# Optimization experiments

Hardware: AMD Instinct MI355X
Metric: run time of the kernel (lower is better)

The kernel has to match this reference:

```python
import jax, jax.numpy as jnp
import numpy as np
from jax import lax

B = 8192
HS = 64        # hidden_size (output channels)
HS4 = HS + 4   # internal channel count (68)
K = 3          # conv kernel size


def setup_inputs() -> dict:
    key = jax.random.key(0)
    ks = jax.random.split(key, 16)
    def n(k, shape, s=1.0):
        return jax.random.normal(k, shape, dtype=jnp.float32) * s
    return {
        "x": n(ks[0], (B, HS, 6, 6)),
        "cell": n(ks[1], (B, 2)),
        "interspace_coord": n(ks[2], (B, 2, 6, 6)),
        "conv1_w": n(ks[3], (HS4, HS4, K, K), 0.05),
        "conv1_b": n(ks[4], (HS4,), 0.05),
        "conv3_w": n(ks[5], (HS4, HS4, K, K), 0.05),
        "conv3_b": n(ks[6], (HS4,), 0.05),
        "lin5_w": n(ks[7], (9 * HS, HS4 * 25), 0.02),
        "lin5_b": n(ks[8], (9 * HS,), 0.02),
        "lin4_w": n(ks[9], (9 * HS, HS4 * 16), 0.02),
        "lin4_b": n(ks[10], (9 * HS,), 0.02),
        "lin3_w": n(ks[11], (9 * HS, HS4 * 9), 0.02),
        "lin3_b": n(ks[12], (9 * HS,), 0.02),
        "final_w": n(ks[13], (HS, 9 * HS), 0.02),
        "final_b": n(ks[14], (HS,), 0.02),
    }


def _conv(z, w, b):
    # torch Conv2d with padding=k//2, stride 1 == SAME conv, NCHW/OIHW
    y = lax.conv_general_dilated(z, w, (1, 1), 'SAME',
                                 dimension_numbers=('NCHW', 'OIHW', 'NCHW'))
    return y + b[None, :, None, None]


def _corners(z, ws):
    # four corner windows, stacked on a new leading axis (corner-major)
    H, W = z.shape[-2:]
    return jnp.stack([z[..., :ws, :ws],
                      z[..., :ws, W - ws:],
                      z[..., H - ws:, :ws],
                      z[..., H - ws:, W - ws:]], axis=0)


def reference(x, cell, interspace_coord,
              conv1_w, conv1_b, conv3_w, conv3_b,
              lin5_w, lin5_b, lin4_w, lin4_b, lin3_w, lin3_b,
              final_w, final_b):
    Bn = x.shape[0]
    new_cell = jnp.broadcast_to(cell.reshape(Bn, -1)[:, :, None, None],
                                (Bn, 2, 6, 6))
    lins = {5: (lin5_w, lin5_b), 4: (lin4_w, lin4_b), 3: (lin3_w, lin3_b)}
    for ws in (5, 4, 3):
        z = jnp.concatenate([x, new_cell, interspace_coord], axis=1)  # [B,68,6,6]
        z = _corners(z, ws).reshape(-1, HS4, ws, ws)                  # [4B,68,ws,ws]
        z = jnp.sin(z) + jnp.cos(z)
        z = jax.nn.relu(_conv(z, conv1_w, conv1_b))
        z = jnp.sin(z) + jnp.cos(z)
        z = jax.nn.relu(_conv(z, conv3_w, conv3_b)).reshape(4, Bn, -1)
        Wl, bl = lins[ws]
        z = jax.nn.relu(z @ Wl.T + bl).reshape(4, Bn, HS, 3, 3)
        m = jnp.concatenate([z[0], z[1]], axis=-1)   # [B,64,3,6]
        n = jnp.concatenate([z[2], z[3]], axis=-1)
        x = jnp.concatenate([m, n], axis=-2)          # [B,64,6,6]
    ew = 3
    c = _corners(x, ew)                               # [4,B,64,3,3]
    c = c.reshape(4 * Bn, -1) @ final_w.T + final_b   # [4B,64]
    c = c.reshape(Bn, HS, 2, 2)                       # same flat-order reshape as torch
    xc = x[:, :, ew - 1:ew + 1, ew - 1:ew + 1]        # center 2x2
    return (xc * c).reshape(Bn, HS, -1)
```

## Files before the change

kernel.cpp:

```cpp
#include <hip/hip_runtime.h>
#include <hip/hip_bf16.h>
#include <cstdint>
#include <cstddef>

#define BN 8192
#define MTOT 32768

using bf16 = __hip_bfloat16;
typedef float f32x4 __attribute__((ext_vector_type(4)));
typedef short short8 __attribute__((ext_vector_type(8)));

__device__ __forceinline__ bf16 f2b(float v) { return __float2bfloat16(v); }
__device__ __forceinline__ float b2f(bf16 v) { return __bfloat162float(v); }
__device__ __forceinline__ float sincos_sum(float x) {
    return 1.41421356237f * __sinf(x + 0.78539816340f);
}


__global__ __launch_bounds__(256)
void zprep_block(const float* __restrict__ xF, const float* __restrict__ cell,
                 const float* __restrict__ isc, bf16* __restrict__ Z,
                 int m0g, int CM)
{
    constexpr int KD = 1728, KTRUE = 1700;
    const int b = blockIdx.x, tid = threadIdx.x;
    __shared__ float s[68][37];

    for (int i = tid; i < 64 * 36; i += 256) {
        int ic = i / 36, off = i % 36;
        s[ic][off] = sincos_sum(xF[((size_t)b * 64 + ic) * 36 + off]);
    }
    if (tid < 2) {
        float t = sincos_sum(cell[b * 2 + tid]);
        #pragma unroll
        for (int off = 0; off < 36; off++) s[64 + tid][off] = t;
    }
    if (tid >= 64 && tid < 136) {
        int j = tid - 64;
        int ic = j / 36, off = j % 36;
        s[66 + ic][off] = sincos_sum(isc[((size_t)b * 2 + ic) * 36 + off]);
    }
    __syncthreads();

    for (int i = tid; i < 4 * KD; i += 256) {
        int q = i / KD, k = i % KD;
        int gm = q * BN + b;
        if (gm < m0g || gm >= m0g + CM) continue;
        float v = 0.f;
        if (k < KTRUE) {
            int pi = k / 68, ic = k % 68;
            int r = (q >> 1) + pi / 5;
            int c = (q & 1) + pi % 5;
            v = s[ic][r * 6 + c];
        }
        Z[(size_t)(gm - m0g) * KD + k] = f2b(v);
    }
}

template<int WSv>
__device__ __forceinline__ bf16 conv_elem(const float* __restrict__ src, int n, int k)
{
    constexpr int KTRUE = 68 * WSv * WSv;
    float v = 0.f;
    if (n < KTRUE && k < KTRUE) {
        int po = n / 68, oc = n % 68, ro = po / WSv, co = po % WSv;
        int pi = k / 68, ic = k % 68, ri = pi / WSv, ci = pi % WSv;
        int kr = ri - ro + 1, kc = ci - co + 1;
        if (kr >= 0 && kr < 3 && kc >= 0 && kc < 3)
            v = src[((oc * 68 + ic) * 3 + kr) * 3 + kc];
    }
    return f2b(v);
}
template<int WSv>
__device__ __forceinline__ bf16 lin_elem(const float* __restrict__ wl, int n, int k)
{
    constexpr int KTRUE = 68 * WSv * WSv;
    float v = 0.f;
    if (n < 576 && k < KTRUE) {
        int pi = k / 68, ic = k % 68;
        v = wl[(size_t)n * KTRUE + ic * (WSv * WSv) + pi];
    }
    return f2b(v);
}

__global__ void megabuild(const float* __restrict__ c1w, const float* __restrict__ c3w,
                          const float* __restrict__ l5w, const float* __restrict__ l4w,
                          const float* __restrict__ l3w, const float* __restrict__ fw,
                          const float* __restrict__ c1b, const float* __restrict__ c3b,
                          const float* __restrict__ bl5, const float* __restrict__ bl4,
                          const float* __restrict__ bl3, const float* __restrict__ bfin,
                          const float* __restrict__ cell, const float* __restrict__ isc,
                          bf16* __restrict__ w1d5, bf16* __restrict__ w3d5,
                          bf16* __restrict__ w1d4, bf16* __restrict__ w3d4,
                          bf16* __restrict__ w1d3, bf16* __restrict__ w3d3,
                          bf16* __restrict__ wl5p, bf16* __restrict__ wl4p,
                          bf16* __restrict__ wl3p, bf16* __restrict__ wfp,
                          float* __restrict__ bias,
                          bf16* __restrict__ Z4, bf16* __restrict__ Z3)
{
    constexpr unsigned S0 = 2u*1792*1728, S1 = 2u*1152*1088, S2 = 2u*640*640;
    constexpr unsigned S3 = 640u*1728, S4 = 640u*1088, S5 = 640u*640;
    constexpr unsigned S6 = 128u*576, S7 = 9216;
    constexpr unsigned S8 = 4u*8192*16*4, S9 = 4u*8192*9*4, S10 = 32768u*28;
    constexpr unsigned O1=S0, O2=O1+S1, O3=O2+S2, O4=O3+S3, O5=O4+S4, O6=O5+S5,
                       O7=O6+S6, O8=O7+S7, O9=O8+S8, O10=O9+S9, OT=O10+S10;
    unsigned e = blockIdx.x * 256u + threadIdx.x;
    if (e >= OT) return;
    if (e < O1) {
        constexpr unsigned per = 1792u*1728;
        unsigned i = (e < per) ? e : e - per;
        bf16* dst = (e < per) ? w1d5 : w3d5;
        const float* src = (e < per) ? c1w : c3w;
        dst[i] = conv_elem<5>(src, (int)(i / 1728u), (int)(i % 1728u));
    } else if (e < O2) {
        unsigned i0 = e - O1; constexpr unsigned per = 1152u*1088;
        unsigned i = (i0 < per) ? i0 : i0 - per;
        bf16* dst = (i0 < per) ? w1d4 : w3d4;
        const float* src = (i0 < per) ? c1w : c3w;
        dst[i] = conv_elem<4>(src, (int)(i / 1088u), (int)(i % 1088u));
    } else if (e < O3) {
        unsigned i0 = e - O2; constexpr unsigned per = 640u*640;
        unsigned i = (i0 < per) ? i0 : i0 - per;
        bf16* dst = (i0 < per) ? w1d3 : w3d3;
        const float* src = (i0 < per) ? c1w : c3w;
        dst[i] = conv_elem<3>(src, (int)(i / 640u), (int)(i % 640u));
    } else if (e < O4) {
        unsigned i = e - O3;
        wl5p[i] = lin_elem<5>(l5w, (int)(i / 1728u), (int)(i % 1728u));
    } else if (e < O5) {
        unsigned i = e - O4;
        wl4p[i] = lin_elem<4>(l4w, (int)(i / 1088u), (int)(i % 1088u));
    } else if (e < O6) {
        unsigned i = e - O5;
        wl3p[i] = lin_elem<3>(l3w, (int)(i / 640u), (int)(i % 640u));
    } else if (e < O7) {
        unsigned i = e - O6, n = i / 576u, k = i % 576u;
        wfp[i] = (n < 64u) ? f2b(fw[n * 576u + k]) : f2b(0.f);
    } else if (e < O8) {
        int i = (int)(e - O7);
        float v = 0.f;
        if (i < 1792)      { int n = i;        if (n < 1700) v = c1b[n % 68]; }
        else if (i < 3584) { int n = i - 1792; if (n < 1700) v = c3b[n % 68]; }
        else if (i < 4736) { int n = i - 3584; if (n < 1088) v = c1b[n % 68]; }
        else if (i < 5888) { int n = i - 4736; if (n < 1088) v = c3b[n % 68]; }
        else if (i < 6528) { int n = i - 5888; if (n < 612)  v = c1b[n % 68]; }
        else if (i < 7168) { int n = i - 6528; if (n < 612)  v = c3b[n % 68]; }
        else if (i < 7808) { int n = i - 7168; if (n < 576)  v = bl5[n]; }
        else if (i < 8448) { int n = i - 7808; if (n < 576)  v = bl4[n]; }
        else if (i < 9088) { int n = i - 8448; if (n < 576)  v = bl3[n]; }
        else               { int n = i - 9088; if (n < 64)   v = bfin[n]; }
        bias[i] = v;
    } else if (e < O9) {
        unsigned i = e - O8;
        int j = (int)(i & 3u); i >>= 2;
        int pi = (int)(i & 15u); i >>= 4;
        int b = (int)(i & 8191u); int q = (int)(i >> 13);
        float t;
        if (j < 2) t = cell[b * 2 + j];
        else {
            int r = (q >> 1) * 2 + pi / 4, c = (q & 1) * 2 + pi % 4;
            t = isc[((size_t)b * 2 + (j - 2)) * 36 + r * 6 + c];
        }
        Z4[((size_t)q * BN + b) * 1088 + pi * 68 + 64 + j] = f2b(sincos_sum(t));
    } else if (e < O10) {
        unsigned i = e - O9;
        int j = (int)(i & 3u); i >>= 2;
        int pi = (int)(i % 9u); i /= 9u;
        int b = (int)(i & 8191u); int q = (int)(i >> 13);
        float t;
        if (j < 2) t = cell[b * 2 + j];
        else {
            int r = (q >> 1) * 3 + pi / 3, c = (q & 1) * 3 + pi % 3;
            t = isc[((size_t)b * 2 + (j - 2)) * 36 + r * 6 + c];
        }
        Z3[((size_t)q * BN + b) * 640 + pi * 68 + 64 + j] = f2b(sincos_sum(t));
    } else {
        unsigned i = e - O10;
        int m = (int)(i / 28u), t = (int)(i % 28u);
        Z3[(size_t)m * 640 + 612 + t] = f2b(0.f);
    }
}

__device__ __forceinline__ void gload_lds16(const bf16* g, const bf16* lds_wave_base)
{
    unsigned off = (unsigned)(uintptr_t)lds_wave_base;
    off = __builtin_amdgcn_readfirstlane(off);
    __builtin_amdgcn_global_load_lds((const __attribute__((address_space(1))) unsigned int*)g,
                                     (__attribute__((address_space(3))) unsigned int*)off,
                                     16, 0, 0);
}

__device__ __forceinline__ int imin(int a, int b) { return a < b ? a : b; }
__device__ __forceinline__ int imax(int a, int b) { return a > b ? a : b; }

template<int EPI, int WS, int WN>
__global__ __launch_bounds__(512, 2)
void gemm8(const bf16* __restrict__ A, const bf16* __restrict__ Bm, int KD,
           const float* __restrict__ bias, int ntiles,
           bf16* __restrict__ C, int ldc, int nlimit,
           int m0g, bf16* __restrict__ znext)
{
    __shared__ bf16 As[3][16384];
    __shared__ bf16 Bs[3][4096];
    const int tid = threadIdx.x;
    const int wave = tid >> 6, lane = tid & 63;
    const int l15 = lane & 15, lq = lane >> 4;
    const int wr = wave * 64;

    const int id = blockIdx.x;
    const int mt8 = (int)gridDim.x / (ntiles * 8);
    const int xcd = id & 7, local = id >> 3;
    const int m_idx = xcd * mt8 + local / ntiles;
    const int n_idx = local % ntiles;
    const int n0 = n_idx * 128, m0 = m_idx * 512;

    int s0b = 0, s0e = KD, s1b = 0, s1e = 0, s2b = 0, s2e = 0;
    if (WS > 0) {
        int po_lo = imin(n0 / 68, WS * WS - 1);
        int po_hi = imin((n0 + 127) / 68, WS * WS - 1);
        int ro_lo = po_lo / WS, ro_hi = po_hi / WS;
        int r_lo = imax(ro_lo - 1, 0), r_hi = imin(ro_hi + 1, WS - 1);
        int ci_lo = 0, ci_hi = WS - 1;
        if (ro_lo == ro_hi) {
            ci_lo = imax(po_lo % WS - 1, 0);
            ci_hi = imin(po_hi % WS + 1, WS - 1);
        }
        if (ci_lo == 0 && ci_hi == WS - 1) {
            s0b = (r_lo * WS * 68) & ~31;
            s0e = imin(KD, ((r_hi + 1) * WS * 68 + 31) & ~31);
        } else {
            s0b = ((r_lo * WS + ci_lo) * 68) & ~31;
            s0e = imin(KD, (((r_lo * WS + ci_hi + 1) * 68) + 31) & ~31);
            if (r_hi > r_lo) {
                s1b = (((r_lo + 1) * WS + ci_lo) * 68) & ~31;
                s1e = imin(KD, ((((r_lo + 1) * WS + ci_hi + 1) * 68) + 31) & ~31);
            }
            if (r_hi > r_lo + 1) {
                s2b = (((r_lo + 2) * WS + ci_lo) * 68) & ~31;
                s2e = imin(KD, ((((r_lo + 2) * WS + ci_hi + 1) * 68) + 31) & ~31);
            }
        }
    }
    const int c0 = (s0e - s0b) >> 5;
    const int c1 = c0 + ((s1e - s1b) >> 5);
    const int nt = c1 + ((s2e - s2b) >> 5);
    auto k0_of = [&](int t2) -> int {
        int k = s0b + (t2 << 5);
        if (t2 >= c0) k = s1b + ((t2 - c0) << 5);
        if (t2 >= c1) k = s2b + ((t2 - c1) << 5);
        return k;
    };

    const int srow = tid >> 2;
    const int sc8 = (tid & 3) ^ ((srow >> 1) & 3);
    const bf16* aSrc = A + (size_t)(m0 + srow) * KD + sc8 * 8;
    const bf16* bSrc = Bm + (size_t)(n0 + srow) * KD + sc8 * 8;
    const int sOff = srow * 32 + (tid & 3) * 8;

    auto stageA01 = [&](int k0, int buf) {
        gload_lds16(aSrc + k0, &As[buf][sOff]);
        gload_lds16(aSrc + k0 + (size_t)128 * KD, &As[buf][sOff + 4096]);
    };
    auto stageA23 = [&](int k0, int buf) {
        gload_lds16(aSrc + k0 + (size_t)256 * KD, &As[buf][sOff + 8192]);
        gload_lds16(aSrc + k0 + (size_t)384 * KD, &As[buf][sOff + 12288]);
    };
    auto stageB = [&](int k0, int buf) {
        gload_lds16(bSrc + k0, &Bs[buf][sOff]);
    };

    const int lrA = wr + l15;
    const int offA0 = lrA * 32 + ((lq ^ ((l15 >> 1) & 3)) * 8);
    const int offB0 = l15 * 32 + ((lq ^ ((l15 >> 1) & 3)) * 8);

    f32x4 acc[4][8];
    #pragma unroll
    for (int i = 0; i < 4; i++)
        #pragma unroll
        for (int j = 0; j < 8; j++) { f32x4 z = {0.f, 0.f, 0.f, 0.f}; acc[i][j] = z; }

    {
        const int k0a = k0_of(0);
        stageA01(k0a, 0); stageA23(k0a, 0); stageB(k0a, 0);
        if (nt > 1) {
            const int k0b = k0_of(1);
            stageA01(k0b, 1); stageA23(k0b, 1); stageB(k0b, 1);
        }
        __syncthreads();
    }

    for (int t = 0; t < nt; ++t) {
        const int cur = t % 3;
        const int nx = (t + 2) % 3;
        const bool pf = (t + 2) < nt;

        const bf16* Ac = &As[cur][0];
        const bf16* Bc = &Bs[cur][0];

        short8 af[4], bg[8];
        #pragma unroll
        for (int i = 0; i < 4; i++) af[i] = *(const short8*)&Ac[offA0 + i * 512];
        #pragma unroll
        for (int j = 0; j < 8; j++) bg[j] = *(const short8*)&Bc[offB0 + j * 512];

        if (pf) {
            const int k2 = k0_of(t + 2);
            stageA01(k2, nx); stageA23(k2, nx); stageB(k2, nx);
        }

        __builtin_amdgcn_s_setprio(1);
        #pragma unroll
        for (int i = 0; i < 4; i++)
            #pragma unroll
            for (int j = 0; j < 8; j++)
                acc[i][j] = __builtin_amdgcn_mfma_f32_16x16x32_bf16(af[i], bg[j], acc[i][j], 0, 0, 0);
        __builtin_amdgcn_s_setprio(0);

        if (pf) asm volatile("s_waitcnt vmcnt(5)" ::: "memory");
        else    asm volatile("s_waitcnt vmcnt(0)" ::: "memory");
        __builtin_amdgcn_s_barrier();
    }

    float bj[8];
    #pragma unroll
    for (int j = 0; j < 8; j++) bj[j] = bias[n0 + j * 16 + l15];

    #pragma unroll
    for (int i = 0; i < 4; i++) {
        #pragma unroll
        for (int j = 0; j < 8; j++) {
            int n = n0 + j * 16 + l15;
            #pragma unroll
            for (int r = 0; r < 4; r++) {
                int m = m0 + wr + i * 16 + lq * 4 + r;
                float v = acc[i][j][r];
                if (EPI == 0) {
                    if (n < nlimit) {
                        v += bj[j]; v = fmaxf(v, 0.f); v = sincos_sum(v);
                        C[(size_t)m * ldc + n] = f2b(v);
                    }
                } else if (EPI == 1) {
                    if (n < nlimit) {
                        v += bj[j]; v = fmaxf(v, 0.f);
                        C[(size_t)m * ldc + n] = f2b(v);
                    }
                } else {
                    if (n < 576) {
                        v += bj[j]; v = fmaxf(v, 0.f);
                        bf16 tv = f2b(sincos_sum(v));
                        int gm = m0g + m;
                        int q = gm >> 13, b = gm & (BN - 1);
                        int ch = n / 9, p = n % 9;
                        int R = p / 3 + (q >> 1) * 3, Cc = p % 3 + (q & 1) * 3;
                        constexpr int OFF = 6 - WN;
                        constexpr int KDN = (WN == 4) ? 1088 : 640;
                        #pragma unroll
                        for (int qr = 0; qr < 2; qr++) {
                            int rr = R - OFF * qr;
                            if (rr < 0 || rr >= WN) continue;
                            #pragma unroll
                            for (int qc = 0; qc < 2; qc++) {
                                int cc = Cc - OFF * qc;
                                if (cc < 0 || cc >= WN) continue;
                                int pi = rr * WN + cc;
                                znext[((size_t)((qr * 2 + qc) * BN + b)) * KDN + pi * 68 + ch] = tv;
                            }
                        }
                    }
                }
            }
        }
    }
}

template<int EPI, int WS, int WN>
__global__ __launch_bounds__(256)
void gemm_bt(const bf16* __restrict__ A, const bf16* __restrict__ Bm, int KD,
             const float* __restrict__ bias, int ntiles,
             bf16* __restrict__ C, int ldc, int nlimit,
             int m0g, bf16* __restrict__ znext,
             const bf16* __restrict__ afin_xc, float* __restrict__ outp)
{
    __shared__ bf16 As[128 * 32];
    __shared__ bf16 Bs[128 * 32];
    const int tid = threadIdx.x;
    const int wave = tid >> 6, lane = tid & 63;
    const int l15 = lane & 15, lq = lane >> 4;
    const int wr = (wave >> 1) * 64, wc = (wave & 1) * 64;

    const int id = blockIdx.x;
    const int mt8 = (int)gridDim.x / (ntiles * 8);
    const int xcd = id & 7, local = id >> 3;
    const int m_idx = xcd * mt8 + local / ntiles;
    const int n_idx = local % ntiles;
    const int n0 = n_idx * 128, m0 = m_idx * 128;

    int nspans = 1, sbeg[4], send[4];
    sbeg[0] = 0; send[0] = KD;
    if (WS > 0) {
        int po_lo = imin(n0 / 68, WS * WS - 1);
        int po_hi = imin((n0 + 127) / 68, WS * WS - 1);
        int ro_lo = po_lo / WS, ro_hi = po_hi / WS;
        int r_lo = imax(ro_lo - 1, 0), r_hi = imin(ro_hi + 1, WS - 1);
        int ci_lo = 0, ci_hi = WS - 1;
        if (ro_lo == ro_hi) {
            ci_lo = imax(po_lo % WS - 1, 0);
            ci_hi = imin(po_hi % WS + 1, WS - 1);
        }
        if (ci_lo == 0 && ci_hi == WS - 1) {
            sbeg[0] = (r_lo * WS * 68) & ~31;
            send[0] = imin(KD, ((r_hi + 1) * WS * 68 + 31) & ~31);
        } else {
            nspans = 0;
            for (int ri = r_lo; ri <= r_hi; ri++) {
                sbeg[nspans] = ((ri * WS + ci_lo) * 68) & ~31;
                send[nspans] = imin(KD, (((ri * WS + ci_hi + 1) * 68) + 31) & ~31);
                nspans++;
            }
        }
    }

    float bj[4];
    #pragma unroll
    for (int j = 0; j < 4; j++) bj[j] = bias[n0 + wc + j * 16 + l15];

    const bf16* Ab = A + (size_t)m0 * KD;
    const bf16* Bb = Bm + (size_t)n0 * KD;
    const int srow = tid >> 2, scol = (tid & 3) * 8;
    const bf16* aG0 = Ab + (size_t)srow * KD + scol;
    const bf16* aG1 = Ab + (size_t)(srow + 64) * KD + scol;
    const bf16* bG0 = Bb + (size_t)srow * KD + scol;
    const bf16* bG1 = Bb + (size_t)(srow + 64) * KD + scol;
    const bf16* lA0 = &As[wave * 512];
    const bf16* lA1 = &As[2048 + wave * 512];
    const bf16* lB0 = &Bs[wave * 512];
    const bf16* lB1 = &Bs[2048 + wave * 512];

    f32x4 acc[4][4];
    #pragma unroll
    for (int i = 0; i < 4; i++)
        #pragma unroll
        for (int j = 0; j < 4; j++) { f32x4 z = {0.f, 0.f, 0.f, 0.f}; acc[i][j] = z; }

    for (int s = 0; s < nspans; s++) {
        for (int k0 = sbeg[s]; k0 < send[s]; k0 += 32) {
            gload_lds16(aG0 + k0, lA0);
            gload_lds16(aG1 + k0, lA1);
            gload_lds16(bG0 + k0, lB0);
            gload_lds16(bG1 + k0, lB1);
            __syncthreads();
            short8 af[4], bg[4];
            #pragma unroll
            for (int i = 0; i < 4; i++) af[i] = *(const short8*)&As[(wr + i * 16 + l15) * 32 + lq * 8];
            #pragma unroll
            for (int j = 0; j < 4; j++) bg[j] = *(const short8*)&Bs[(wc + j * 16 + l15) * 32 + lq * 8];
            #pragma unroll
            for (int i = 0; i < 4; i++)
                #pragma unroll
                for (int j = 0; j < 4; j++)
                    acc[i][j] = __builtin_amdgcn_mfma_f32_16x16x32_bf16(af[i], bg[j], acc[i][j], 0, 0, 0);
            __syncthreads();
        }
    }

    #pragma unroll
    for (int i = 0; i < 4; i++) {
        #pragma unroll
        for (int j = 0; j < 4; j++) {
            int n = n0 + wc + j * 16 + l15;
            #pragma unroll
            for (int r = 0; r < 4; r++) {
                int m = m0 + wr + i * 16 + lq * 4 + r;
                float v = acc[i][j][r];
                if (EPI == 0) {
                    if (n < nlimit) {
                        v += bj[j]; v = fmaxf(v, 0.f); v = sincos_sum(v);
                        C[(size_t)m * ldc + n] = f2b(v);
                    }
                } else if (EPI == 1) {
                    if (n < nlimit) {
                        v += bj[j]; v = fmaxf(v, 0.f);
                        C[(size_t)m * ldc + n] = f2b(v);
                    }
                } else if (EPI == 2) {
                    if (n < 576) {
                        v += bj[j]; v = fmaxf(v, 0.f);
                        bf16 t = f2b(sincos_sum(v));
                        int gm = m0g + m;
                        int q = gm >> 13, b = gm & (BN - 1);
                        int ch = n / 9, p = n % 9;
                        int R = p / 3 + (q >> 1) * 3, Cc = p % 3 + (q & 1) * 3;
                        constexpr int OFF = 6 - WN;
                        constexpr int KDN = (WN == 4) ? 1088 : 640;
                        #pragma unroll
                        for (int qr = 0; qr < 2; qr++) {
                            int rr = R - OFF * qr;
                            if (rr < 0 || rr >= WN) continue;
                            #pragma unroll
                            for (int qc = 0; qc < 2; qc++) {
                                int cc = Cc - OFF * qc;
                                if (cc < 0 || cc >= WN) continue;
                                int pi = rr * WN + cc;
                                znext[((size_t)((qr * 2 + qc) * BN + b)) * KDN + pi * 68 + ch] = t;
                            }
                        }
                    }
                } else {
                    if (n < 64) {
                        v += bj[j];
                        int gm = m0g + m;
                        int f = gm * 64 + n;
                        int b2 = f >> 8, rem = f & 255;
                        int ch2 = rem >> 2, ii = (rem >> 1) & 1, jj = rem & 1;
                        int qq = ii * 2 + jj;
                        const int offt[4] = {8, 6, 2, 0};
                        float xc = b2f(afin_xc[((size_t)qq * BN + b2) * 576 + ch2 * 9 + offt[qq]]);
                        outp[f] = v * xc;
                    }
                }
            }
        }
    }
}

extern "C" void kernel_launch(void* const* d_in, const int* in_sizes, int n_in,
                              void* d_out, int out_size, void* d_ws, size_t ws_size,
                              hipStream_t stream)
{
    const float* x    = (const float*)d_in[0];
    const float* cell = (const float*)d_in[1];
    const float* isc  = (const float*)d_in[2];
    const float* c1w  = (const float*)d_in[3];
    const float* c1b  = (const float*)d_in[4];
    const float* c3w  = (const float*)d_in[5];
    const float* c3b  = (const float*)d_in[6];
    const float* l5w  = (const float*)d_in[7];
    const float* l5b  = (const float*)d_in[8];
    const float* l4w  = (const float*)d_in[9];
    const float* l4b  = (const float*)d_in[10];
    const float* l3w  = (const float*)d_in[11];
    const float* l3b  = (const float*)d_in[12];
    const float* fw   = (const float*)d_in[13];
    const float* fb   = (const float*)d_in[14];

    char* base = (char*)d_ws;
    size_t cur = 0;
    auto take = [&](size_t bytes) -> char* {
        char* r = base + cur; cur += (bytes + 255) & ~(size_t)255; return r;
    };

    const size_t Z4B = (size_t)MTOT * 1088 * 2;
    const size_t Z3B = (size_t)MTOT * 640 * 2;
    const size_t AFB = (size_t)MTOT * 576 * 2;
    size_t wbytes = 2 * (1792ull * 1728 + 1152ull * 1088 + 640ull * 640) * 2
                  + (640ull * 1728 + 640ull * 1088 + 640ull * 640) * 2
                  + 128ull * 576 * 2 + 9216ull * 4 + 64 * 256;
    auto need = [&](int nc) -> size_t {
        return Z4B + Z3B + AFB + wbytes + 2 * ((size_t)(MTOT / nc) * 1728 * 2);
    };
    const bool use8 = (ws_size >= need(8));
    int nchunk = use8 ? ((ws_size >= need(1)) ? 1 : (ws_size >= need(2)) ? 2
                       : (ws_size >= need(4)) ? 4 : 8)
                      : 16;

    bf16* Z4   = (bf16*)take(Z4B);
    bf16* Z3   = (bf16*)take(Z3B);
    bf16* afinb = (bf16*)take(AFB);
    bf16* w1d5 = (bf16*)take(1792ull * 1728 * 2);
    bf16* w3d5 = (bf16*)take(1792ull * 1728 * 2);
    bf16* w1d4 = (bf16*)take(1152ull * 1088 * 2);
    bf16* w3d4 = (bf16*)take(1152ull * 1088 * 2);
    bf16* w1d3 = (bf16*)take(640ull * 640 * 2);
    bf16* w3d3 = (bf16*)take(640ull * 640 * 2);
    bf16* wl5p = (bf16*)take(640ull * 1728 * 2);
    bf16* wl4p = (bf16*)take(640ull * 1088 * 2);
    bf16* wl3p = (bf16*)take(640ull * 640 * 2);
    bf16* wfp  = (bf16*)take(128ull * 576 * 2);
    float* biasb = (float*)take(9216ull * 4);
    int CM = MTOT / nchunk;
    int mt = CM / 128;
    int mt5 = CM / 512;
    bf16* Za = (bf16*)take((size_t)CM * 1728 * 2);
    bf16* Zb = (bf16*)take((size_t)CM * 1728 * 2);

    {
        constexpr unsigned OT = 2u*1792*1728 + 2u*1152*1088 + 2u*640*640
                              + 640u*1728 + 640u*1088 + 640u*640 + 128u*576 + 9216
                              + 4u*8192*16*4 + 4u*8192*9*4 + 32768u*28;
        megabuild<<<(OT + 255) / 256, 256, 0, stream>>>(
            c1w, c3w, l5w, l4w, l3w, fw, c1b, c3b, l5b, l4b, l3b, fb, cell, isc,
            w1d5, w3d5, w1d4, w3d4, w1d3, w3d3, wl5p, wl4p, wl3p, wfp, biasb, Z4, Z3);
    }

    if (use8) {
        for (int c = 0; c < nchunk; c++) {
            int m0g = c * CM;
            zprep_block<<<BN, 256, 0, stream>>>(x, cell, isc, Za, m0g, CM);
            gemm8<0, 5, 0><<<14 * mt5, 512, 0, stream>>>(Za, w1d5, 1728, biasb + 0, 14,
                                                         Zb, 1728, 1728, 0, nullptr);
            gemm8<1, 5, 0><<<14 * mt5, 512, 0, stream>>>(Zb, w3d5, 1728, biasb + 1792, 14,
                                                         Za, 1728, 1728, 0, nullptr);
            gemm8<2, 0, 4><<<5 * mt5, 512, 0, stream>>>(Za, wl5p, 1728, biasb + 7168, 5,
                                                        nullptr, 0, 0, m0g, Z4);
        }
        for (int c = 0; c < nchunk; c++) {
            int m0g = c * CM;
            gemm8<0, 4, 0><<<9 * mt5, 512, 0, stream>>>(Z4 + (size_t)m0g * 1088, w1d4, 1088,
                                                        biasb + 3584, 9, Zb, 1088, 1088,
                                                        0, nullptr);
            gemm8<1, 4, 0><<<9 * mt5, 512, 0, stream>>>(Zb, w3d4, 1088, biasb + 4736, 9,
                                                        Za, 1088, 1088, 0, nullptr);
            gemm8<2, 0, 3><<<5 * mt5, 512, 0, stream>>>(Za, wl4p, 1088, biasb + 7808, 5,
                                                        nullptr, 0, 0, m0g, Z3);
        }
        for (int c = 0; c < nchunk; c++) {
            int m0g = c * CM;
            gemm8<0, 3, 0><<<5 * mt5, 512, 0, stream>>>(Z3 + (size_t)m0g * 640, w1d3, 640,
                                                        biasb + 5888, 5, Zb, 640, 640,
                                                        0, nullptr);
            gemm8<1, 3, 0><<<5 * mt5, 512, 0, stream>>>(Zb, w3d3, 640, biasb + 6528, 5,
                                                        Za, 640, 640, 0, nullptr);
            gemm8<1, 0, 0><<<5 * mt5, 512, 0, stream>>>(Za, wl3p, 640, biasb + 8448, 5,
                                                        afinb + (size_t)m0g * 576, 576, 576,
                                                        0, nullptr);
        }
    } else {
        for (int c = 0; c < nchunk; c++) {
            int m0g = c * CM;
            zprep_block<<<BN, 256, 0, stream>>>(x, cell, isc, Za, m0g, CM);
            gemm_bt<0, 5, 0><<<14 * mt, 256, 0, stream>>>(Za, w1d5, 1728, biasb + 0, 14,
                                                          Zb, 1728, 1728, 0, nullptr, nullptr, nullptr);
            gemm_bt<1, 5, 0><<<14 * mt, 256, 0, stream>>>(Zb, w3d5, 1728, biasb + 1792, 14,
                                                          Za, 1728, 1728, 0, nullptr, nullptr, nullptr);
            gemm_bt<2, 0, 4><<<5 * mt, 256, 0, stream>>>(Za, wl5p, 1728, biasb + 7168, 5,
                                                         nullptr, 0, 0, m0g, Z4, nullptr, nullptr);
        }
        for (int c = 0; c < nchunk; c++) {
            int m0g = c * CM;
            gemm_bt<0, 4, 0><<<9 * mt, 256, 0, stream>>>(Z4 + (size_t)m0g * 1088, w1d4, 1088,
                                                         biasb + 3584, 9, Zb, 1088, 1088,
                                                         0, nullptr, nullptr, nullptr);
            gemm_bt<1, 4, 0><<<9 * mt, 256, 0, stream>>>(Zb, w3d4, 1088, biasb + 4736, 9,
                                                         Za, 1088, 1088, 0, nullptr, nullptr, nullptr);
            gemm_bt<2, 0, 3><<<5 * mt, 256, 0, stream>>>(Za, wl4p, 1088, biasb + 7808, 5,
                                                         nullptr, 0, 0, m0g, Z3, nullptr, nullptr);
        }
        for (int c = 0; c < nchunk; c++) {
            int m0g = c * CM;
            gemm_bt<0, 3, 0><<<5 * mt, 256, 0, stream>>>(Z3 + (size_t)m0g * 640, w1d3, 640,
                                                         biasb + 5888, 5, Zb, 640, 640,
                                                         0, nullptr, nullptr, nullptr);
            gemm_bt<1, 3, 0><<<5 * mt, 256, 0, stream>>>(Zb, w3d3, 640, biasb + 6528, 5,
                                                         Za, 640, 640, 0, nullptr, nullptr, nullptr);
            gemm_bt<1, 0, 0><<<5 * mt, 256, 0, stream>>>(Za, wl3p, 640, biasb + 8448, 5,
                                                         afinb + (size_t)m0g * 576, 576, 576,
                                                         0, nullptr, nullptr, nullptr);
        }
    }
    for (int c = 0; c < nchunk; c++) {
        int m0g = c * CM;
        gemm_bt<3, 0, 0><<<mt, 256, 0, stream>>>(afinb + (size_t)m0g * 576, wfp, 576,
                                                 biasb + 9088, 1, nullptr, 0, 0, m0g,
                                                 nullptr, afinb, (float*)d_out);
    }
}
```

Baseline: 1.322 ms.

## Shrink gemm8 tile to 256x128 with 2x4 wave grid and always use it

Changes the gemm8 block tile from 512x128 (8 waves stacked in M) to 256x128, with the waves arranged 4x2 so each computes a 64x64 sub-tile. This halves LDS and accumulator use per block, raising launch_bounds occupancy to 4 blocks per CU and doubling the grid size. It also removes the gemm_bt fallback path so gemm8 runs for every chunk count, and updates the vmcnt wait for the smaller number of loads per stage. In exchange, each wave reuses less A data per B fragment, and a smaller workspace now goes through gemm8 as well.

```diff
diff --git a/kernel.cpp b/kernel.cpp
--- a/kernel.cpp
+++ b/kernel.cpp
@@ -194,25 +194,25 @@
 __device__ __forceinline__ int imax(int a, int b) { return a > b ? a : b; }
 
 template<int EPI, int WS, int WN>
-__global__ __launch_bounds__(512, 2)
+__global__ __launch_bounds__(512, 4)
 void gemm8(const bf16* __restrict__ A, const bf16* __restrict__ Bm, int KD,
            const float* __restrict__ bias, int ntiles,
            bf16* __restrict__ C, int ldc, int nlimit,
            int m0g, bf16* __restrict__ znext)
 {
-    __shared__ bf16 As[3][16384];
+    __shared__ bf16 As[3][8192];
     __shared__ bf16 Bs[3][4096];
     const int tid = threadIdx.x;
     const int wave = tid >> 6, lane = tid & 63;
     const int l15 = lane & 15, lq = lane >> 4;
-    const int wr = wave * 64;
+    const int wr = (wave >> 1) * 64, wc = (wave & 1) * 64;
 
     const int id = blockIdx.x;
     const int mt8 = (int)gridDim.x / (ntiles * 8);
     const int xcd = id & 7, local = id >> 3;
     const int m_idx = xcd * mt8 + local / ntiles;
     const int n_idx = local % ntiles;
-    const int n0 = n_idx * 128, m0 = m_idx * 512;
+    const int n0 = n_idx * 128, m0 = m_idx * 256;
 
     int s0b = 0, s0e = KD, s1b = 0, s1e = 0, s2b = 0, s2e = 0;
     if (WS > 0) {
@@ -257,34 +257,30 @@
     const bf16* bSrc = Bm + (size_t)(n0 + srow) * KD + sc8 * 8;
     const int sOff = srow * 32 + (tid & 3) * 8;
 
-    auto stageA01 = [&](int k0, int buf) {
+    auto stageA = [&](int k0, int buf) {
         gload_lds16(aSrc + k0, &As[buf][sOff]);
         gload_lds16(aSrc + k0 + (size_t)128 * KD, &As[buf][sOff + 4096]);
-    };
-    auto stageA23 = [&](int k0, int buf) {
-        gload_lds16(aSrc + k0 + (size_t)256 * KD, &As[buf][sOff + 8192]);
-        gload_lds16(aSrc + k0 + (size_t)384 * KD, &As[buf][sOff + 12288]);
     };
     auto stageB = [&](int k0, int buf) {
         gload_lds16(bSrc + k0, &Bs[buf][sOff]);
     };
 
-    const int lrA = wr + l15;
-    const int offA0 = lrA * 32 + ((lq ^ ((l15 >> 1) & 3)) * 8);
-    const int offB0 = l15 * 32 + ((lq ^ ((l15 >> 1) & 3)) * 8);
-
-    f32x4 acc[4][8];
+    const int swz = (lq ^ ((l15 >> 1) & 3)) * 8;
+    const int offA0 = (wr + l15) * 32 + swz;
+    const int offB0 = (wc + l15) * 32 + swz;
+
+    f32x4 acc[4][4];
     #pragma unroll
     for (int i = 0; i < 4; i++)
         #pragma unroll
-        for (int j = 0; j < 8; j++) { f32x4 z = {0.f, 0.f, 0.f, 0.f}; acc[i][j] = z; }
+        for (int j = 0; j < 4; j++) { f32x4 z = {0.f, 0.f, 0.f, 0.f}; acc[i][j] = z; }
 
     {
         const int k0a = k0_of(0);
-        stageA01(k0a, 0); stageA23(k0a, 0); stageB(k0a, 0);
+        stageA(k0a, 0); stageB(k0a, 0);
         if (nt > 1) {
             const int k0b = k0_of(1);
-            stageA01(k0b, 1); stageA23(k0b, 1); stageB(k0b, 1);
+            stageA(k0b, 1); stageB(k0b, 1);
         }
         __syncthreads();
     }
@@ -297,39 +293,39 @@
         const bf16* Ac = &As[cur][0];
         const bf16* Bc = &Bs[cur][0];
 
-        short8 af[4], bg[8];
+        short8 af[4], bg[4];
         #pragma unroll
         for (int i = 0; i < 4; i++) af[i] = *(const short8*)&Ac[offA0 + i * 512];
         #pragma unroll
-        for (int j = 0; j < 8; j++) bg[j] = *(const short8*)&Bc[offB0 + j * 512];
+        for (int j = 0; j < 4; j++) bg[j] = *(const short8*)&Bc[offB0 + j * 512];
 
         if (pf) {
             const int k2 = k0_of(t + 2);
-            stageA01(k2, nx); stageA23(k2, nx); stageB(k2, nx);
+            stageA(k2, nx); stageB(k2, nx);
         }
 
         __builtin_amdgcn_s_setprio(1);
         #pragma unroll
         for (int i = 0; i < 4; i++)
             #pragma unroll
-            for (int j = 0; j < 8; j++)
+            for (int j = 0; j < 4; j++)
                 acc[i][j] = __builtin_amdgcn_mfma_f32_16x16x32_bf16(af[i], bg[j], acc[i][j], 0, 0, 0);
         __builtin_amdgcn_s_setprio(0);
 
-        if (pf) asm volatile("s_waitcnt vmcnt(5)" ::: "memory");
+        if (pf) asm volatile("s_waitcnt vmcnt(3)" ::: "memory");
         else    asm volatile("s_waitcnt vmcnt(0)" ::: "memory");
         __builtin_amdgcn_s_barrier();
     }
 
-    float bj[8];
+    float bj[4];
     #pragma unroll
-    for (int j = 0; j < 8; j++) bj[j] = bias[n0 + j * 16 + l15];
+    for (int j = 0; j < 4; j++) bj[j] = bias[n0 + wc + j * 16 + l15];
 
     #pragma unroll
     for (int i = 0; i < 4; i++) {
         #pragma unroll
-        for (int j = 0; j < 8; j++) {
-            int n = n0 + j * 16 + l15;
+        for (int j = 0; j < 4; j++) {
+            int n = n0 + wc + j * 16 + l15;
             #pragma unroll
             for (int r = 0; r < 4; r++) {
                 int m = m0 + wr + i * 16 + lq * 4 + r;
@@ -558,10 +554,8 @@
     auto need = [&](int nc) -> size_t {
         return Z4B + Z3B + AFB + wbytes + 2 * ((size_t)(MTOT / nc) * 1728 * 2);
     };
-    const bool use8 = (ws_size >= need(8));
-    int nchunk = use8 ? ((ws_size >= need(1)) ? 1 : (ws_size >= need(2)) ? 2
-                       : (ws_size >= need(4)) ? 4 : 8)
-                      : 16;
+    int nchunk = (ws_size >= need(1)) ? 1 : (ws_size >= need(2)) ? 2
+               : (ws_size >= need(4)) ? 4 : (ws_size >= need(8)) ? 8 : 16;
 
     bf16* Z4   = (bf16*)take(Z4B);
     bf16* Z3   = (bf16*)take(Z3B);
@@ -579,7 +573,7 @@
     float* biasb = (float*)take(9216ull * 4);
     int CM = MTOT / nchunk;
     int mt = CM / 128;
-    int mt5 = CM / 512;
+    int mt2 = CM / 256;
     bf16* Za = (bf16*)take((size_t)CM * 1728 * 2);
     bf16* Zb = (bf16*)take((size_t)CM * 1728 * 2);
 
@@ -592,70 +586,36 @@
             w1d5, w3d5, w1d4, w3d4, w1d3, w3d3, wl5p, wl4p, wl3p, wfp, biasb, Z4, Z3);
     }
 
-    if (use8) {
-        for (int c = 0; c < nchunk; c++) {
-            int m0g = c * CM;
-            zprep_block<<<BN, 256, 0, stream>>>(x, cell, isc, Za, m0g, CM);
-            gemm8<0, 5, 0><<<14 * mt5, 512, 0, stream>>>(Za, w1d5, 1728, biasb + 0, 14,
-                                                         Zb, 1728, 1728, 0, nullptr);
-            gemm8<1, 5, 0><<<14 * mt5, 512, 0, stream>>>(Zb, w3d5, 1728, biasb + 1792, 14,
-                                                         Za, 1728, 1728, 0, nullptr);
-            gemm8<2, 0, 4><<<5 * mt5, 512, 0, stream>>>(Za, wl5p, 1728, biasb + 7168, 5,
-                                                        nullptr, 0, 0, m0g, Z4);
-        }
-        for (int c = 0; c < nchunk; c++) {
-            int m0g = c * CM;
-            gemm8<0, 4, 0><<<9 * mt5, 512, 0, stream>>>(Z4 + (size_t)m0g * 1088, w1d4, 1088,
-                                                        biasb + 3584, 9, Zb, 1088, 1088,
-                                                        0, nullptr);
-            gemm8<1, 4, 0><<<9 * mt5, 512, 0, stream>>>(Zb, w3d4, 1088, biasb + 4736, 9,
-                                                        Za, 1088, 1088, 0, nullptr);
-            gemm8<2, 0, 3><<<5 * mt5, 512, 0, stream>>>(Za, wl4p, 1088, biasb + 7808, 5,
-                                                        nullptr, 0, 0, m0g, Z3);
-        }
-        for (int c = 0; c < nchunk; c++) {
-            int m0g = c * CM;
-            gemm8<0, 3, 0><<<5 * mt5, 512, 0, stream>>>(Z3 + (size_t)m0g * 640, w1d3, 640,
-                                                        biasb + 5888, 5, Zb, 640, 640,
-                                                        0, nullptr);
-            gemm8<1, 3, 0><<<5 * mt5, 512, 0, stream>>>(Zb, w3d3, 640, biasb + 6528, 5,
-                                                        Za, 640, 640, 0, nullptr);
-            gemm8<1, 0, 0><<<5 * mt5, 512, 0, stream>>>(Za, wl3p, 640, biasb + 8448, 5,
-                                                        afinb + (size_t)m0g * 576, 576, 576,
-                                                        0, nullptr);
-        }
-    } else {
-        for (int c = 0; c < nchunk; c++) {
-            int m0g = c * CM;
-            zprep_block<<<BN, 256, 0, stream>>>(x, cell, isc, Za, m0g, CM);
-            gemm_bt<0, 5, 0><<<14 * mt, 256, 0, stream>>>(Za, w1d5, 1728, biasb + 0, 14,
-                                                          Zb, 1728, 1728, 0, nullptr, nullptr, nullptr);
-            gemm_bt<1, 5, 0><<<14 * mt, 256, 0, stream>>>(Zb, w3d5, 1728, biasb + 1792, 14,
-                                                          Za, 1728, 1728, 0, nullptr, nullptr, nullptr);
-            gemm_bt<2, 0, 4><<<5 * mt, 256, 0, stream>>>(Za, wl5p, 1728, biasb + 7168, 5,
-                                                         nullptr, 0, 0, m0g, Z4, nullptr, nullptr);
-        }
-        for (int c = 0; c < nchunk; c++) {
-            int m0g = c * CM;
-            gemm_bt<0, 4, 0><<<9 * mt, 256, 0, stream>>>(Z4 + (size_t)m0g * 1088, w1d4, 1088,
-                                                         biasb + 3584, 9, Zb, 1088, 1088,
-                                                         0, nullptr, nullptr, nullptr);
-            gemm_bt<1, 4, 0><<<9 * mt, 256, 0, stream>>>(Zb, w3d4, 1088, biasb + 4736, 9,
-                                                         Za, 1088, 1088, 0, nullptr, nullptr, nullptr);
-            gemm_bt<2, 0, 3><<<5 * mt, 256, 0, stream>>>(Za, wl4p, 1088, biasb + 7808, 5,
-                                                         nullptr, 0, 0, m0g, Z3, nullptr, nullptr);
-        }
-        for (int c = 0; c < nchunk; c++) {
-            int m0g = c * CM;
-            gemm_bt<0, 3, 0><<<5 * mt, 256, 0, stream>>>(Z3 + (size_t)m0g * 640, w1d3, 640,
-                                                         biasb + 5888, 5, Zb, 640, 640,
-                                                         0, nullptr, nullptr, nullptr);
-            gemm_bt<1, 3, 0><<<5 * mt, 256, 0, stream>>>(Zb, w3d3, 640, biasb + 6528, 5,
-                                                         Za, 640, 640, 0, nullptr, nullptr, nullptr);
-            gemm_bt<1, 0, 0><<<5 * mt, 256, 0, stream>>>(Za, wl3p, 640, biasb + 8448, 5,
-                                                         afinb + (size_t)m0g * 576, 576, 576,
-                                                         0, nullptr, nullptr, nullptr);
-        }
+    for (int c = 0; c < nchunk; c++) {
+        int m0g = c * CM;
+        zprep_block<<<BN, 256, 0, stream>>>(x, cell, isc, Za, m0g, CM);
+        gemm8<0, 5, 0><<<14 * mt2, 512, 0, stream>>>(Za, w1d5, 1728, biasb + 0, 14,
+                                                     Zb, 1728, 1728, 0, nullptr);
+        gemm8<1, 5, 0><<<14 * mt2, 512, 0, stream>>>(Zb, w3d5, 1728, biasb + 1792, 14,
+                                                     Za, 1728, 1728, 0, nullptr);
+        gemm8<2, 0, 4><<<5 * mt2, 512, 0, stream>>>(Za, wl5p, 1728, biasb + 7168, 5,
+                                                    nullptr, 0, 0, m0g, Z4);
+    }
+    for (int c = 0; c < nchunk; c++) {
+        int m0g = c * CM;
+        gemm8<0, 4, 0><<<9 * mt2, 512, 0, stream>>>(Z4 + (size_t)m0g * 1088, w1d4, 1088,
+                                                    biasb + 3584, 9, Zb, 1088, 1088,
+                                                    0, nullptr);
+        gemm8<1, 4, 0><<<9 * mt2, 512, 0, stream>>>(Zb, w3d4, 1088, biasb + 4736, 9,
+                                                    Za, 1088, 1088, 0, nullptr);
+        gemm8<2, 0, 3><<<5 * mt2, 512, 0, stream>>>(Za, wl4p, 1088, biasb + 7808, 5,
+                                                    nullptr, 0, 0, m0g, Z3);
+    }
+    for (int c = 0; c < nchunk; c++) {
+        int m0g = c * CM;
+        gemm8<0, 3, 0><<<5 * mt2, 512, 0, stream>>>(Z3 + (size_t)m0g * 640, w1d3, 640,
+                                                    biasb + 5888, 5, Zb, 640, 640,
+                                                    0, nullptr);
+        gemm8<1, 3, 0><<<5 * mt2, 512, 0, stream>>>(Zb, w3d3, 640, biasb + 6528, 5,
+                                                    Za, 640, 640, 0, nullptr);
+        gemm8<1, 0, 0><<<5 * mt2, 512, 0, stream>>>(Za, wl3p, 640, biasb + 8448, 5,
+                                                    afinb + (size_t)m0g * 576, 576, 576,
+                                                    0, nullptr);
     }
     for (int c = 0; c < nchunk; c++) {
         int m0g = c * CM;
```

Result: faster. 1.228 ms (-7.1%).
